# Kernel tuning notes

Hardware: AMD Instinct MI355X
Metric: run time of the kernel (lower is better)

The kernel has to match this reference:

```python
import jax, jax.numpy as jnp
import numpy as np
from jax import lax

T = 131072  # num frames
PARENTS = [-1, 0, 0, 1, 2, 3, 4, 5, 6]          # lower-body kinematic tree
LOWER_BODY = [0, 1, 2, 4, 5, 7, 8, 10, 11]      # SMPL joint ids of the 9 lower-body joints
FEET = [7, 5, 8, 6]                              # left toe, left heel, right toe, right heel (lower-body local ids)
FLOOR_Y = -0.93                                  # min y of ankle/foot joints in SMPL zero pose
GRAVITY_VELOCITY = -0.0018


def setup_inputs() -> dict:
    key = jax.random.key(0)
    k1, k2, k3 = jax.random.split(key, 3)
    pose = jax.random.normal(k1, (T, 24, 3, 3), dtype=jnp.float32)
    bone = 0.2 * jax.random.normal(k2, (9, 3), dtype=jnp.float32)
    bone = bone.at[:3].set(0.0)  # root + hip offsets zeroed, as in __init__ (b[:3] = 0)
    index = jax.random.randint(k3, (T,), 0, 4, dtype=jnp.int32)
    return {"pose": pose, "lower_body_bone": bone, "index": index}


def _forward_kinematics(pose_lower, bone):
    # pose_lower: [T, 9, 3, 3] local rotations; bone: [9, 3] bone offsets.
    # R_global[i] = R_global[parent] @ R_local[i];  p[i] = p[parent] + R_global[parent] @ bone[i]
    Rg = [pose_lower[:, 0]]
    p = [jnp.broadcast_to(bone[0], (pose_lower.shape[0], 3))]
    for i in range(1, 9):
        pa = PARENTS[i]
        Rg.append(jnp.einsum('tij,tjk->tik', Rg[pa], pose_lower[:, i]))
        p.append(p[pa] + jnp.einsum('tij,j->ti', Rg[pa], bone[i]))
    return jnp.stack(p, axis=1)  # [T, 9, 3]


def reference(pose, lower_body_bone, index):
    gravity = jnp.array([0.0, GRAVITY_VELOCITY, 0.0], dtype=pose.dtype)
    pose_lower = pose[:, jnp.array(LOWER_BODY)]               # [T, 9, 3, 3]
    j = _forward_kinematics(pose_lower, lower_body_bone)      # [T, 9, 3]

    # per-foot velocities: j[t-1] - j[t], zero at t=0  -> [T, 4, 3]
    feet = j[:, jnp.array(FEET)]                              # [T, 4, 3]
    vel_full = jnp.concatenate([jnp.zeros((1, 4, 3), dtype=j.dtype), feet[:-1] - feet[1:]], axis=0)
    vel_select = jnp.take_along_axis(vel_full, index[:, None, None].astype(jnp.int32), axis=1)[:, 0]  # [T, 3]
    velocity = gravity + vel_select                           # [T, 3]

    # sequential floor-contact correction on the y component
    foot_min_y = jnp.min(j[:, 5:9, 1], axis=1)                # [T]

    def step(root_y, inp):
        vy, fmin = inp
        foot_y = root_y + fmin
        vy_new = jnp.where(foot_y + vy <= FLOOR_Y, FLOOR_Y - foot_y, vy)
        return root_y + vy_new, vy_new

    _, vy_all = lax.scan(step, jnp.asarray(0.0, dtype=j.dtype), (velocity[:, 1], foot_min_y))
    velocity = velocity.at[:, 1].set(vy_all)

    trans = jnp.cumsum(velocity, axis=0)                      # velocity_to_root_position
    return pose, trans
```

## Files before the change

kernel.cpp:

```cpp
#include <hip/hip_runtime.h>
#include <math.h>

#define T_TOTAL   131072
#define POSE_FLTS (131072 * 216)
#define BT        64
#define NU        (T_TOTAL / BT)
#define F4PB      (BT * 54)
#define TILE_W    65
#define TILE_F    72
#define SCR       (TILE_F * TILE_W)
#define FLOOR_YC  (-0.93f)
#define GRAV_Y    (-0.0018f)
#define NEG_INF   (-INFINITY)

typedef float floatx4 __attribute__((ext_vector_type(4)));


__device__ __forceinline__ void mat3mul(const float* A, const float* B, float* C) {
#pragma unroll
    for (int r = 0; r < 3; ++r) {
#pragma unroll
        for (int c = 0; c < 3; ++c) {
            C[r * 3 + c] = fmaf(A[r * 3 + 2], B[6 + c],
                           fmaf(A[r * 3 + 1], B[3 + c],
                                A[r * 3 + 0] * B[c]));
        }
    }
}

__device__ __forceinline__ void mva(const float* R, const float* b,
                                    const float* pin, float* pout) {
#pragma unroll
    for (int r = 0; r < 3; ++r) {
        pout[r] = pin[r] + fmaf(R[r * 3 + 2], b[2],
                            fmaf(R[r * 3 + 1], b[1], R[r * 3 + 0] * b[0]));
    }
}

__device__ __forceinline__ float sel_foot(const float f[12], int idx, int c) {
    float r = f[0 + c];
    r = (idx == 1) ? f[3 + c] : r;
    r = (idx == 2) ? f[6 + c] : r;
    r = (idx == 3) ? f[9 + c] : r;
    return r;
}

__device__ __forceinline__ void fk_core(const float* Pl,
                                        const float* __restrict__ bone,
                                        float feet[12], float* fmin) {
    const float* M0 = Pl + 0;
    const float* M1 = Pl + 9;
    const float* M2 = Pl + 18;
    const float* M3 = Pl + 28;
    const float* M4 = Pl + 37;
    const float* M5 = Pl + 51;
    const float* M6 = Pl + 60;

    float R1[9], R2[9], R3[9], R4[9], R5[9], R6[9];
    mat3mul(M0, M1, R1);
    mat3mul(M0, M2, R2);
    mat3mul(R1, M3, R3);
    mat3mul(R2, M4, R4);
    mat3mul(R3, M5, R5);
    mat3mul(R4, M6, R6);

    float p0[3] = {bone[0], bone[1], bone[2]};
    float p1[3], p2[3], p3[3], p4a[3], p5[3], p6[3], p7[3], p8[3];
    mva(M0, bone + 3,  p0, p1);
    mva(M0, bone + 6,  p0, p2);
    mva(R1, bone + 9,  p1, p3);
    mva(R2, bone + 12, p2, p4a);
    mva(R3, bone + 15, p3, p5);
    mva(R4, bone + 18, p4a, p6);
    mva(R5, bone + 21, p5, p7);
    mva(R6, bone + 24, p6, p8);

    feet[0] = p7[0]; feet[1]  = p7[1]; feet[2]  = p7[2];
    feet[3] = p5[0]; feet[4]  = p5[1]; feet[5]  = p5[2];
    feet[6] = p8[0]; feet[7]  = p8[1]; feet[8]  = p8[2];
    feet[9] = p6[0]; feet[10] = p6[1]; feet[11] = p6[2];
    *fmin = fminf(fminf(p5[1], p6[1]), fminf(p7[1], p8[1]));
}

__device__ __forceinline__ void fk_feet_col(const float* __restrict__ tile, int col,
                                            const float* __restrict__ bone,
                                            float feet[12], float* fmin) {
    float Pl[TILE_F];
#pragma unroll
    for (int f = 0; f < TILE_F; ++f) Pl[f] = tile[f * TILE_W + col];
    fk_core(Pl, bone, feet, fmin);
}

__device__ __forceinline__ void wave_incl_scan(float& Sx, float& Sz,
                                               float& A, float& B, int lane) {
#pragma unroll
    for (int off = 1; off < 64; off <<= 1) {
        float ox = __shfl_up(Sx, off, 64);
        float oz = __shfl_up(Sz, off, 64);
        float oA = __shfl_up(A, off, 64);
        float oB = __shfl_up(B, off, 64);
        if (lane >= off) {
            Sx += ox;
            Sz += oz;
            B = fmaxf(oB + A, B);
            A = oA + A;
        }
    }
}

__device__ __forceinline__ void extract_tile(float* __restrict__ tile, int idx, floatx4 q) {
    int tsl = idx / 54;
    int w   = idx - tsl * 54;
    int base = -1;
    if (w <= 6)                  base = 4 * w;
    else if (w >= 9 && w <= 13)  base = 4 * w - 8;
    else if (w >= 15 && w <= 20) base = 4 * w - 12;
    if (base >= 0) {
        tile[(base + 0) * TILE_W + tsl] = q.x;
        tile[(base + 1) * TILE_W + tsl] = q.y;
        tile[(base + 2) * TILE_W + tsl] = q.z;
        tile[(base + 3) * TILE_W + tsl] = q.w;
    }
}


__global__ __launch_bounds__(256) void k_main(const float* __restrict__ pose,
                                              const float* __restrict__ bone,
                                              const int* __restrict__ index,
                                              floatx4* __restrict__ outPose4,
                                              float4* __restrict__ vws,
                                              float4* __restrict__ wsAgg) {
    __shared__ __align__(16) float tile[SCR + 16];
    int tid = threadIdx.x, u = blockIdx.x;

    const floatx4* __restrict__ src = (const floatx4*)pose + (size_t)u * F4PB;
    floatx4*       __restrict__ dst = outPose4              + (size_t)u * F4PB;

    floatx4 r[14];
#pragma unroll
    for (int j = 0; j < 13; ++j) r[j] = src[j * 256 + tid];
    floatx4 qb;
    bool has14   = (tid < 128);
    bool hasBnd  = (u > 0 && tid >= 128 && tid < 128 + 18);
    if (has14) {
        r[13] = src[13 * 256 + tid];
    } else if (hasBnd) {
        int k = tid - 128;
        int o = k + (k >= 7 ? 2 : 0) + (k >= 12 ? 1 : 0);
        qb = *(const floatx4*)(pose + ((size_t)u * BT - 1) * 216 + o * 4);
    }

#pragma unroll
    for (int j = 0; j < 13; ++j) {
        int idx = j * 256 + tid;
        __builtin_nontemporal_store(r[j], &dst[idx]);
        extract_tile(tile, idx, r[j]);
    }
    if (has14) {
        int idx = 13 * 256 + tid;
        __builtin_nontemporal_store(r[13], &dst[idx]);
        extract_tile(tile, idx, r[13]);
    } else if (hasBnd) {
        int k = tid - 128;
#pragma unroll
        for (int i = 0; i < 4; ++i) tile[(4 * k + i) * TILE_W + 64] = qb[i];
    }
    __syncthreads();

    float feet[12], fmin = 0.f;
    if (tid < 64) {
        fk_feet_col(tile, tid, bone, feet, &fmin);
    } else if (tid == 64 && u > 0) {
        float f2[12], m2;
        fk_feet_col(tile, 64, bone, f2, &m2);
#pragma unroll
        for (int k = 0; k < 12; ++k) tile[SCR + k] = f2[k];
    }
    __syncthreads();

    if (tid < 64) {
        int lane = tid;
        int t = u * BT + lane;

        float fp[12];
#pragma unroll
        for (int k = 0; k < 12; ++k) fp[k] = __shfl_up(feet[k], 1, 64);
        if (lane == 0 && u > 0) {
#pragma unroll
            for (int k = 0; k < 12; ++k) fp[k] = tile[SCR + k];
        }

        float vx, vy, vz;
        if (t == 0) {
            vx = 0.f; vy = GRAV_Y; vz = 0.f;
        } else {
            int idx = index[t];
            vx = sel_foot(fp, idx, 0) - sel_foot(feet, idx, 0);
            vy = GRAV_Y + sel_foot(fp, idx, 1) - sel_foot(feet, idx, 1);
            vz = sel_foot(fp, idx, 2) - sel_foot(feet, idx, 2);
        }
        float ix = vx, iz = vz, iA = vy, iB = FLOOR_YC - fmin;
        wave_incl_scan(ix, iz, iA, iB, lane);

        vws[(size_t)t] = make_float4(ix, iz, iA, iB);
        if (lane == 63) wsAgg[u] = make_float4(ix, iz, iA, iB);
    }
}

__global__ __launch_bounds__(1024) void k_phase2(const float4* __restrict__ wsAgg,
                                                 float4* __restrict__ wsIn) {
    __shared__ float sx[1024], sz[1024], sa[1024], sb[1024];
    int tid = threadIdx.x;

    float4 a0 = wsAgg[2 * tid];
    float4 a1 = wsAgg[2 * tid + 1];
    float cx = a0.x + a1.x;
    float cz = a0.y + a1.y;
    float cb = fmaxf(a0.w + a1.z, a1.w);
    float ca = a0.z + a1.z;
    sx[tid] = cx; sz[tid] = cz; sa[tid] = ca; sb[tid] = cb;
    __syncthreads();

    for (int off = 1; off < 1024; off <<= 1) {
        float px = 0.f, pz = 0.f, pa = 0.f, pb = NEG_INF;
        bool h = (tid >= off);
        if (h) { px = sx[tid - off]; pz = sz[tid - off]; pa = sa[tid - off]; pb = sb[tid - off]; }
        __syncthreads();
        if (h) {
            float qa = sa[tid], qb = sb[tid];
            sx[tid] = px + sx[tid];
            sz[tid] = pz + sz[tid];
            sb[tid] = fmaxf(pb + qa, qb);
            sa[tid] = pa + qa;
        }
        __syncthreads();
    }

    float ex = 0.f, ez = 0.f, ea = 0.f, eb = NEG_INF;
    if (tid > 0) { ex = sx[tid - 1]; ez = sz[tid - 1]; ea = sa[tid - 1]; eb = sb[tid - 1]; }

    wsIn[2 * tid] = make_float4(ex, ez, fmaxf(ea, eb), 0.f);

    float fx = ex + a0.x;
    float fz = ez + a0.y;
    float fb = fmaxf(eb + a0.z, a0.w);
    float fa = ea + a0.z;
    wsIn[2 * tid + 1] = make_float4(fx, fz, fmaxf(fa, fb), 0.f);
}

__global__ __launch_bounds__(256) void k_phase3(const float4* __restrict__ vws,
                                                const float4* __restrict__ wsIn,
                                                float* __restrict__ trans) {
    int tid = threadIdx.x, bk = blockIdx.x;
    int lane = tid & 63, wv = tid >> 6;
    int u = bk * 4 + wv;
    size_t t = (size_t)u * 64 + lane;

    float4 v   = vws[t];
    float4 bin = wsIn[u];
    trans[t * 3 + 0] = bin.x + v.x;
    trans[t * 3 + 1] = fmaxf(bin.z + v.z, v.w);
    trans[t * 3 + 2] = bin.y + v.y;
}


extern "C" void kernel_launch(void* const* d_in, const int* in_sizes, int n_in,
                              void* d_out, int out_size, void* d_ws, size_t ws_size,
                              hipStream_t stream) {
    const float* pose  = (const float*)d_in[0];
    const float* bone  = (const float*)d_in[1];
    const int*   index = (const int*)d_in[2];
    float* out   = (float*)d_out;
    float* trans = out + POSE_FLTS;

    float4* vws   = (float4*)d_ws;
    float4* wsAgg = vws + T_TOTAL;
    float4* wsIn  = wsAgg + NU;

    k_main  <<<NU, 256, 0, stream>>>(pose, bone, index, (floatx4*)out, vws, wsAgg);
    k_phase2<<<1, 1024, 0, stream>>>(wsAgg, wsIn);
    k_phase3<<<NU / 4, 256, 0, stream>>>(vws, wsIn, trans);
}
```

Before: 51.74 us.

## Split pose copy across waves and fold block-prefix scan into apply kernel

In k_main, threads now load only the 24 rotation float4s per frame that are needed for forward kinematics and stage them into the LDS tile. Wave 0 then runs FK and the wave scan while the other three waves copy the remaining 30 float4s per frame to the output. Wave 0 also computes the boundary frame itself, which removes one __syncthreads. The single-block phase-2 scan is removed: every k_apply block redundantly scans all 2048 block aggregates from wsAgg to get its own prefixes, so one kernel launch goes away. The trade-offs are repeated scan work in every apply block and integer division for address computation.

```diff
diff --git a/kernel.cpp b/kernel.cpp
--- a/kernel.cpp
+++ b/kernel.cpp
@@ -130,51 +130,39 @@
                                               floatx4* __restrict__ outPose4,
                                               float4* __restrict__ vws,
                                               float4* __restrict__ wsAgg) {
-    __shared__ __align__(16) float tile[SCR + 16];
+    __shared__ __align__(16) float tile[SCR + 4];
     int tid = threadIdx.x, u = blockIdx.x;
 
     const floatx4* __restrict__ src = (const floatx4*)pose + (size_t)u * F4PB;
     floatx4*       __restrict__ dst = outPose4              + (size_t)u * F4PB;
 
-    floatx4 r[14];
-#pragma unroll
-    for (int j = 0; j < 13; ++j) r[j] = src[j * 256 + tid];
+    floatx4 a[6];
+    int ai[6];
+#pragma unroll
+    for (int j = 0; j < 6; ++j) {
+        int r  = j * 256 + tid;
+        int ts = r / 24;
+        int w  = r - ts * 24;
+        ai[j]  = ts * 54 + w;
+        a[j]   = src[ai[j]];
+    }
     floatx4 qb;
-    bool has14   = (tid < 128);
-    bool hasBnd  = (u > 0 && tid >= 128 && tid < 128 + 18);
-    if (has14) {
-        r[13] = src[13 * 256 + tid];
-    } else if (hasBnd) {
+    bool hasBnd = (u > 0 && tid >= 128 && tid < 128 + 18);
+    if (hasBnd) {
         int k = tid - 128;
         int o = k + (k >= 7 ? 2 : 0) + (k >= 12 ? 1 : 0);
         qb = *(const floatx4*)(pose + ((size_t)u * BT - 1) * 216 + o * 4);
     }
 
 #pragma unroll
-    for (int j = 0; j < 13; ++j) {
-        int idx = j * 256 + tid;
-        __builtin_nontemporal_store(r[j], &dst[idx]);
-        extract_tile(tile, idx, r[j]);
-    }
-    if (has14) {
-        int idx = 13 * 256 + tid;
-        __builtin_nontemporal_store(r[13], &dst[idx]);
-        extract_tile(tile, idx, r[13]);
-    } else if (hasBnd) {
+    for (int j = 0; j < 6; ++j) {
+        __builtin_nontemporal_store(a[j], &dst[ai[j]]);
+        extract_tile(tile, ai[j], a[j]);
+    }
+    if (hasBnd) {
         int k = tid - 128;
 #pragma unroll
         for (int i = 0; i < 4; ++i) tile[(4 * k + i) * TILE_W + 64] = qb[i];
-    }
-    __syncthreads();
-
-    float feet[12], fmin = 0.f;
-    if (tid < 64) {
-        fk_feet_col(tile, tid, bone, feet, &fmin);
-    } else if (tid == 64 && u > 0) {
-        float f2[12], m2;
-        fk_feet_col(tile, 64, bone, f2, &m2);
-#pragma unroll
-        for (int k = 0; k < 12; ++k) tile[SCR + k] = f2[k];
     }
     __syncthreads();
 
@@ -182,12 +170,21 @@
         int lane = tid;
         int t = u * BT + lane;
 
+        float feet[12], fmin;
+        fk_feet_col(tile, lane, bone, feet, &fmin);
+
+        float fb[12];
+        if (lane == 0 && u > 0) {
+            float mb;
+            fk_feet_col(tile, 64, bone, fb, &mb);
+        }
+
         float fp[12];
 #pragma unroll
         for (int k = 0; k < 12; ++k) fp[k] = __shfl_up(feet[k], 1, 64);
         if (lane == 0 && u > 0) {
 #pragma unroll
-            for (int k = 0; k < 12; ++k) fp[k] = tile[SCR + k];
+            for (int k = 0; k < 12; ++k) fp[k] = fb[k];
         }
 
         float vx, vy, vz;
@@ -204,60 +201,86 @@
 
         vws[(size_t)t] = make_float4(ix, iz, iA, iB);
         if (lane == 63) wsAgg[u] = make_float4(ix, iz, iA, iB);
-    }
-}
-
-__global__ __launch_bounds__(1024) void k_phase2(const float4* __restrict__ wsAgg,
-                                                 float4* __restrict__ wsIn) {
-    __shared__ float sx[1024], sz[1024], sa[1024], sb[1024];
-    int tid = threadIdx.x;
-
-    float4 a0 = wsAgg[2 * tid];
-    float4 a1 = wsAgg[2 * tid + 1];
-    float cx = a0.x + a1.x;
-    float cz = a0.y + a1.y;
-    float cb = fmaxf(a0.w + a1.z, a1.w);
-    float ca = a0.z + a1.z;
-    sx[tid] = cx; sz[tid] = cz; sa[tid] = ca; sb[tid] = cb;
-    __syncthreads();
-
-    for (int off = 1; off < 1024; off <<= 1) {
-        float px = 0.f, pz = 0.f, pa = 0.f, pb = NEG_INF;
-        bool h = (tid >= off);
-        if (h) { px = sx[tid - off]; pz = sz[tid - off]; pa = sa[tid - off]; pb = sb[tid - off]; }
-        __syncthreads();
-        if (h) {
-            float qa = sa[tid], qb = sb[tid];
-            sx[tid] = px + sx[tid];
-            sz[tid] = pz + sz[tid];
-            sb[tid] = fmaxf(pb + qa, qb);
-            sa[tid] = pa + qa;
-        }
-        __syncthreads();
-    }
-
-    float ex = 0.f, ez = 0.f, ea = 0.f, eb = NEG_INF;
-    if (tid > 0) { ex = sx[tid - 1]; ez = sz[tid - 1]; ea = sa[tid - 1]; eb = sb[tid - 1]; }
-
-    wsIn[2 * tid] = make_float4(ex, ez, fmaxf(ea, eb), 0.f);
-
-    float fx = ex + a0.x;
-    float fz = ez + a0.y;
-    float fb = fmaxf(eb + a0.z, a0.w);
-    float fa = ea + a0.z;
-    wsIn[2 * tid + 1] = make_float4(fx, fz, fmaxf(fa, fb), 0.f);
-}
-
-__global__ __launch_bounds__(256) void k_phase3(const float4* __restrict__ vws,
-                                                const float4* __restrict__ wsIn,
-                                                float* __restrict__ trans) {
+    } else {
+        int tt = tid - 64;
+#pragma unroll
+        for (int bat = 0; bat < 2; ++bat) {
+            floatx4 b[5];
+            int bi[5];
+#pragma unroll
+            for (int j = 0; j < 5; ++j) {
+                int r  = (bat * 5 + j) * 192 + tt;
+                int ts = r / 30;
+                int w  = 24 + (r - ts * 30);
+                bi[j]  = ts * 54 + w;
+                b[j]   = src[bi[j]];
+            }
+#pragma unroll
+            for (int j = 0; j < 5; ++j)
+                __builtin_nontemporal_store(b[j], &dst[bi[j]]);
+        }
+    }
+}
+
+
+__global__ __launch_bounds__(256) void k_apply(const float4* __restrict__ wsAgg,
+                                               const float4* __restrict__ vws,
+                                               float* __restrict__ trans) {
+    __shared__ float4 wtot[4];
+    __shared__ float4 pre[4];
     int tid = threadIdx.x, bk = blockIdx.x;
     int lane = tid & 63, wv = tid >> 6;
-    int u = bk * 4 + wv;
-    size_t t = (size_t)u * 64 + lane;
-
-    float4 v   = vws[t];
-    float4 bin = wsIn[u];
+
+    float4 a[8];
+#pragma unroll
+    for (int k = 0; k < 8; ++k) a[k] = wsAgg[tid * 8 + k];
+    float cx = a[0].x, cz = a[0].y, ca = a[0].z, cb = a[0].w;
+#pragma unroll
+    for (int k = 1; k < 8; ++k) {
+        cb = fmaxf(cb + a[k].z, a[k].w);
+        ca += a[k].z;
+        cx += a[k].x; cz += a[k].y;
+    }
+
+    float sx = cx, sz = cz, sa = ca, sb = cb;
+    wave_incl_scan(sx, sz, sa, sb, lane);
+    if (lane == 63) wtot[wv] = make_float4(sx, sz, sa, sb);
+
+    float ex = __shfl_up(sx, 1, 64);
+    float ez = __shfl_up(sz, 1, 64);
+    float eA = __shfl_up(sa, 1, 64);
+    float eB = __shfl_up(sb, 1, 64);
+    if (lane == 0) { ex = 0.f; ez = 0.f; eA = 0.f; eB = NEG_INF; }
+    __syncthreads();
+
+    float wx = 0.f, wz = 0.f, wA = 0.f, wB = NEG_INF;
+    for (int w = 0; w < wv; ++w) {
+        float4 c = wtot[w];
+        wx += c.x; wz += c.y;
+        wB = fmaxf(wB + c.z, c.w);
+        wA += c.z;
+    }
+    float tx = wx + ex, tz = wz + ez;
+    float tB = fmaxf(wB + eA, eB);
+    float tA = wA + eA;
+
+    if (tid == (bk >> 1)) {
+        int j0 = bk * 4 - tid * 8;
+        float px = tx, pz = tz, pA = tA, pB = tB;
+#pragma unroll
+        for (int k = 0; k < 8; ++k) {
+            if (k >= j0 && k < j0 + 4)
+                pre[k - j0] = make_float4(px, pz, fmaxf(pA, pB), 0.f);
+            pB = fmaxf(pB + a[k].z, a[k].w);
+            pA += a[k].z;
+            px += a[k].x; pz += a[k].y;
+        }
+    }
+    __syncthreads();
+
+    float4 bin = pre[wv];
+    size_t t = ((size_t)bk * 4 + wv) * 64 + lane;
+    float4 v = vws[t];
     trans[t * 3 + 0] = bin.x + v.x;
     trans[t * 3 + 1] = fmaxf(bin.z + v.z, v.w);
     trans[t * 3 + 2] = bin.y + v.y;
@@ -276,8 +299,8 @@
     float4* vws   = (float4*)d_ws;
     float4* wsAgg = vws + T_TOTAL;
     float4* wsIn  = wsAgg + NU;
-
-    k_main  <<<NU, 256, 0, stream>>>(pose, bone, index, (floatx4*)out, vws, wsAgg);
-    k_phase2<<<1, 1024, 0, stream>>>(wsAgg, wsIn);
-    k_phase3<<<NU / 4, 256, 0, stream>>>(vws, wsIn, trans);
-}
+    (void)wsIn; (void)ws_size; (void)n_in; (void)in_sizes; (void)out_size;
+
+    k_main <<<NU, 256, 0, stream>>>(pose, bone, index, (floatx4*)out, vws, wsAgg);
+    k_apply<<<NU / 4, 256, 0, stream>>>(wsAgg, vws, trans);
+}
```

New measurement: 51.86 us. About the same (+0.2%).
